# Kernel optimization log

Measured on AMD Instinct MI355X. Metric: run time of the kernel, lower is better.

## Reference

```python
import jax, jax.numpy as jnp
import numpy as np

PROP_TIME = 3
# (top,bottom),(left,right) zero-pad widths for the 8 neighbor shifts,
# matching torch ZeroPad2d((left,right,top,bottom)) in the original module.
PADS = [((0, 2), (0, 2)), ((0, 2), (1, 1)), ((0, 2), (2, 0)),
        ((1, 1), (0, 2)),                   ((1, 1), (2, 0)),
        ((2, 0), (0, 2)), ((2, 0), (1, 1)), ((2, 0), (2, 0))]


def _pad8(x, axis):
    """Pad last two dims 8 ways, stack the copies on `axis`."""
    lead = [(0, 0)] * (x.ndim - 2)
    return jnp.stack([jnp.pad(x, lead + [tb, lr]) for (tb, lr) in PADS], axis=axis)


def _affinity_norm(g):
    # g: [N, 8, H, W] -> gate_wb [N, 8, H+2, W+2], gate_sum [N, H, W]
    gw = jnp.stack([jnp.pad(g[:, k], [(0, 0), PADS[k][0], PADS[k][1]])
                    for k in range(8)], axis=1)
    abs_w = jnp.sum(jnp.abs(gw), axis=1, keepdims=True)
    gw = gw / abs_w
    gsum = jnp.sum(gw, axis=1)[:, 1:-1, 1:-1]
    return gw, gsum


def _propagate_once(gw, gsum, blur):
    # gw: [N,8,H+2,W+2], gsum: [N,H,W], blur: [N,B,H,W]
    nb = _pad8(blur, axis=1)                                # [N,8,B,H+2,W+2]
    ws = jnp.sum(gw[:, :, None] * nb, axis=1)[:, :, 1:-1, 1:-1]  # [N,B,H,W]
    return (1.0 - gsum[:, None]) * blur + ws


def _forward(guidance, blur, prop_time):
    # guidance: [24, X, Y, Z], blur: [B, X, Y, Z]
    gwx, gsx = _affinity_norm(jnp.transpose(guidance[0:8],   (3, 0, 1, 2)))  # [Z,8,X,Y]
    gwy, gsy = _affinity_norm(jnp.transpose(guidance[8:16],  (2, 0, 1, 3)))  # [Y,8,X,Z]
    gwz, gsz = _affinity_norm(jnp.transpose(guidance[16:24], (1, 0, 2, 3)))  # [X,8,Y,Z]
    r = blur
    for _ in range(prop_time):
        r = jnp.transpose(_propagate_once(gwx, gsx, jnp.transpose(r, (3, 0, 1, 2))), (1, 2, 3, 0))
        r = jnp.transpose(_propagate_once(gwy, gsy, jnp.transpose(r, (2, 0, 1, 3))), (1, 2, 0, 3))
        r = jnp.transpose(_propagate_once(gwz, gsz, jnp.transpose(r, (1, 0, 2, 3))), (1, 0, 2, 3))
    return r


def setup_inputs() -> dict:
    key = jax.random.key(0)
    k1, k2 = jax.random.split(key)
    guidance = jax.random.normal(k1, (24, 256, 256, 32), dtype=jnp.float32)
    blur = jax.random.normal(k2, (1, 256, 256, 32), dtype=jnp.float32)
    return {"guidance": guidance, "blur": blur}


def reference(guidance, blur):
    return _forward(guidance, blur, PROP_TIME)
```

## Files before the change

kernel.cpp:

```cpp
#include <hip/hip_runtime.h>


constexpr int X = 256, Y = 256, Z = 32;
constexpr int NV = X * Y * Z;
constexpr int YZ = Y * Z;

__device__ __forceinline__ float4 zero4() { return make_float4(0.f, 0.f, 0.f, 0.f); }

__device__ __forceinline__ void accum(const float4 gk, const float4 rk,
                                      float* asum, float* gsum, float* acc) {
    asum[0] += fabsf(gk.x); gsum[0] += gk.x; acc[0] = fmaf(gk.x, rk.x, acc[0]);
    asum[1] += fabsf(gk.y); gsum[1] += gk.y; acc[1] = fmaf(gk.y, rk.y, acc[1]);
    asum[2] += fabsf(gk.z); gsum[2] += gk.z; acc[2] = fmaf(gk.z, rk.z, acc[2]);
    asum[3] += fabsf(gk.w); gsum[3] += gk.w; acc[3] = fmaf(gk.w, rk.w, acc[3]);
}

template <int DIR>
__global__ __launch_bounds__(256) void prop4(const float* __restrict__ g,
                                             const float* __restrict__ rin,
                                             float* __restrict__ rout) {
    const int t  = blockIdx.x * 256 + threadIdx.x;
    const int f0 = t << 2;
    const int z  = f0 & (Z - 1);
    const int y  = (f0 >> 5) & (Y - 1);
    const int x  = f0 >> 13;

    constexpr int d1[8] = {1, 1, 1, 0, 0, -1, -1, -1};
    constexpr int d2[8] = {1, 0, -1, 1, -1, 1, 0, -1};

    const float* gc = g + DIR * 8 * NV;
    const float4 rc = *(const float4*)(rin + f0);
    float asum[4] = {0, 0, 0, 0}, gsum[4] = {0, 0, 0, 0}, acc[4] = {0, 0, 0, 0};

    if (DIR == 0) {
#pragma unroll
        for (int k = 0; k < 8; ++k) {
            const int a = x + d1[k], b = y + d2[k];
            if (a >= 0 && a < X && b >= 0 && b < Y) {
                const int ofs = f0 + d1[k] * YZ + d2[k] * Z;
                const float4 gv = *(const float4*)(gc + k * NV + ofs);
                const float4 rv = *(const float4*)(rin + ofs);
                accum(gv, rv, asum, gsum, acc);
            }
        }
    } else {
        const int s1 = (DIR == 1) ? YZ : Z;
        const int c1 = (DIR == 1) ? x : y;

        float4 rv[3]; float rl[3], rr[3];
#pragma unroll
        for (int j = 0; j < 3; ++j) {
            const int dd = 1 - j;
            const bool v = (c1 + dd >= 0) && (c1 + dd < 256);
            const float* p = rin + f0 + dd * s1;
            rv[j] = v ? *(const float4*)p : zero4();
            rl[j] = (v && z > 0)     ? p[-1] : 0.f;
            rr[j] = (v && z < Z - 4) ? p[4]  : 0.f;
        }

#pragma unroll
        for (int k = 0; k < 8; ++k) {
            const int j = 1 - d1[k];
            const bool v = (c1 + d1[k] >= 0) && (c1 + d1[k] < 256);
            const float* p = gc + k * NV + f0 + d1[k] * s1;
            const float4 gv = v ? *(const float4*)p : zero4();
            float4 gk, rk;
            if (d2[k] == 1) {
                const float s = (v && z < Z - 4) ? p[4] : 0.f;
                gk = make_float4(gv.y, gv.z, gv.w, s);
                rk = make_float4(rv[j].y, rv[j].z, rv[j].w, rr[j]);
            } else if (d2[k] == -1) {
                const float s = (v && z > 0) ? p[-1] : 0.f;
                gk = make_float4(s, gv.x, gv.y, gv.z);
                rk = make_float4(rl[j], rv[j].x, rv[j].y, rv[j].z);
            } else {
                gk = gv; rk = rv[j];
            }
            accum(gk, rk, asum, gsum, acc);
        }
    }

    float4 o;
    o.x = rc.x + (acc[0] - gsum[0] * rc.x) / asum[0];
    o.y = rc.y + (acc[1] - gsum[1] * rc.y) / asum[1];
    o.z = rc.z + (acc[2] - gsum[2] * rc.z) / asum[2];
    o.w = rc.w + (acc[3] - gsum[3] * rc.w) / asum[3];
    *(float4*)(rout + f0) = o;
}

extern "C" void kernel_launch(void* const* d_in, const int* in_sizes, int n_in,
                              void* d_out, int out_size, void* d_ws, size_t ws_size,
                              hipStream_t stream) {
    const float* g    = (const float*)d_in[0];
    const float* blur = (const float*)d_in[1];
    float* out = (float*)d_out;
    float* ws  = (float*)d_ws;

    const dim3 grid(NV / 1024), block(256);

    const float* src = blur;
    int step = 0;
    for (int it = 0; it < 3; ++it) {
        for (int dir = 0; dir < 3; ++dir) {
            float* dst = (step & 1) ? ws : out;
            switch (dir) {
                case 0: prop4<0><<<grid, block, 0, stream>>>(g, src, dst); break;
                case 1: prop4<1><<<grid, block, 0, stream>>>(g, src, dst); break;
                case 2: prop4<2><<<grid, block, 0, stream>>>(g, src, dst); break;
            }
            src = dst;
            ++step;
        }
    }
}
```

Measured before the change: 375.3 us.

## Fuse nine propagation launches into one cooperative kernel with grid sync

Replaces the nine separate per-direction kernel launches with a single cooperative kernel of 256 blocks that loops over all steps, separated by grid-wide syncs, and falls back to per-step launches if the cooperative launch fails. Conditional loads become clamped unconditional loads with masking, the accumulation is rewritten as g*(r_neighbor - r_center) so the separate gate sum is dropped, and division is replaced by a hardware reciprocal. The goal is to remove launch overhead and branchy memory access, but only 256 blocks with one block per CU limits occupancy for a memory-bound stencil, and the approximate reciprocal slightly changes numerics.

After: 872.3 us. 132% more time.

```diff
diff --git a/kernel.cpp b/kernel.cpp
--- a/kernel.cpp
+++ b/kernel.cpp
@@ -1,91 +1,134 @@
 #include <hip/hip_runtime.h>
+#include <hip/hip_cooperative_groups.h>
+
+namespace cg = cooperative_groups;
 
 
 constexpr int X = 256, Y = 256, Z = 32;
 constexpr int NV = X * Y * Z;
 constexpr int YZ = Y * Z;
+constexpr int GEND = 24 * NV;
 
-__device__ __forceinline__ float4 zero4() { return make_float4(0.f, 0.f, 0.f, 0.f); }
-
-__device__ __forceinline__ void accum(const float4 gk, const float4 rk,
-                                      float* asum, float* gsum, float* acc) {
-    asum[0] += fabsf(gk.x); gsum[0] += gk.x; acc[0] = fmaf(gk.x, rk.x, acc[0]);
-    asum[1] += fabsf(gk.y); gsum[1] += gk.y; acc[1] = fmaf(gk.y, rk.y, acc[1]);
-    asum[2] += fabsf(gk.z); gsum[2] += gk.z; acc[2] = fmaf(gk.z, rk.z, acc[2]);
-    asum[3] += fabsf(gk.w); gsum[3] += gk.w; acc[3] = fmaf(gk.w, rk.w, acc[3]);
+__device__ __forceinline__ int iclamp(int v, int lo, int hi) {
+    return min(max(v, lo), hi);
 }
 
 template <int DIR>
-__global__ __launch_bounds__(256) void prop4(const float* __restrict__ g,
-                                             const float* __restrict__ rin,
-                                             float* __restrict__ rout) {
-    const int t  = blockIdx.x * 256 + threadIdx.x;
-    const int f0 = t << 2;
-    const int z  = f0 & (Z - 1);
-    const int y  = (f0 >> 5) & (Y - 1);
-    const int x  = f0 >> 13;
-
+__device__ __forceinline__ void do_group(int f0, const float* __restrict__ g,
+                                         const float* __restrict__ src,
+                                         float* __restrict__ dst) {
     constexpr int d1[8] = {1, 1, 1, 0, 0, -1, -1, -1};
     constexpr int d2[8] = {1, 0, -1, 1, -1, 1, 0, -1};
+    const int z = f0 & 31, y = (f0 >> 5) & 255, x = f0 >> 13;
+    const int gb0 = DIR * 8 * NV;
 
-    const float* gc = g + DIR * 8 * NV;
-    const float4 rc = *(const float4*)(rin + f0);
-    float asum[4] = {0, 0, 0, 0}, gsum[4] = {0, 0, 0, 0}, acc[4] = {0, 0, 0, 0};
+    float asx = 0, asy = 0, asz = 0, asw = 0;
+    float dx = 0, dy = 0, dz = 0, dw = 0;
+    float4 rc;
 
     if (DIR == 0) {
+        rc = *(const float4*)(src + f0);
 #pragma unroll
         for (int k = 0; k < 8; ++k) {
             const int a = x + d1[k], b = y + d2[k];
-            if (a >= 0 && a < X && b >= 0 && b < Y) {
-                const int ofs = f0 + d1[k] * YZ + d2[k] * Z;
-                const float4 gv = *(const float4*)(gc + k * NV + ofs);
-                const float4 rv = *(const float4*)(rin + ofs);
-                accum(gv, rv, asum, gsum, acc);
-            }
+            const bool valid = ((unsigned)a < 256u) & ((unsigned)b < 256u);
+            const int ofs = f0 + d1[k] * YZ + d2[k] * Z;
+            const float4 rv = *(const float4*)(src + iclamp(ofs, 0, NV - 4));
+            float4 gv = *(const float4*)(g + iclamp(gb0 + k * NV + ofs, 0, GEND - 4));
+            if (!valid) { gv.x = 0.f; gv.y = 0.f; gv.z = 0.f; gv.w = 0.f; }
+            asx += fabsf(gv.x); asy += fabsf(gv.y);
+            asz += fabsf(gv.z); asw += fabsf(gv.w);
+            dx = fmaf(gv.x, rv.x - rc.x, dx); dy = fmaf(gv.y, rv.y - rc.y, dy);
+            dz = fmaf(gv.z, rv.z - rc.z, dz); dw = fmaf(gv.w, rv.w - rc.w, dw);
         }
     } else {
         const int s1 = (DIR == 1) ? YZ : Z;
         const int c1 = (DIR == 1) ? x : y;
-
         float4 rv[3]; float rl[3], rr[3];
 #pragma unroll
         for (int j = 0; j < 3; ++j) {
-            const int dd = 1 - j;
-            const bool v = (c1 + dd >= 0) && (c1 + dd < 256);
-            const float* p = rin + f0 + dd * s1;
-            rv[j] = v ? *(const float4*)p : zero4();
-            rl[j] = (v && z > 0)     ? p[-1] : 0.f;
-            rr[j] = (v && z < Z - 4) ? p[4]  : 0.f;
+            const int ro = f0 + (1 - j) * s1;
+            rv[j] = *(const float4*)(src + iclamp(ro, 0, NV - 4));
+            rl[j] = src[iclamp(ro - 1, 0, NV - 1)];
+            rr[j] = src[iclamp(ro + 4, 0, NV - 1)];
         }
-
+        rc = rv[1];
+        const bool zlo = (z > 0), zhi = (z < Z - 4);
 #pragma unroll
         for (int k = 0; k < 8; ++k) {
             const int j = 1 - d1[k];
-            const bool v = (c1 + d1[k] >= 0) && (c1 + d1[k] < 256);
-            const float* p = gc + k * NV + f0 + d1[k] * s1;
-            const float4 gv = v ? *(const float4*)p : zero4();
+            const bool vrow = (unsigned)(c1 + d1[k]) < 256u;
+            const int gb = gb0 + k * NV + f0 + d1[k] * s1;
+            float4 gv = *(const float4*)(g + iclamp(gb, 0, GEND - 4));
+            if (!vrow) { gv.x = 0.f; gv.y = 0.f; gv.z = 0.f; gv.w = 0.f; }
             float4 gk, rk;
             if (d2[k] == 1) {
-                const float s = (v && z < Z - 4) ? p[4] : 0.f;
-                gk = make_float4(gv.y, gv.z, gv.w, s);
+                float ge = g[iclamp(gb + 4, 0, GEND - 1)];
+                ge = (vrow && zhi) ? ge : 0.f;
+                gk = make_float4(gv.y, gv.z, gv.w, ge);
                 rk = make_float4(rv[j].y, rv[j].z, rv[j].w, rr[j]);
             } else if (d2[k] == -1) {
-                const float s = (v && z > 0) ? p[-1] : 0.f;
-                gk = make_float4(s, gv.x, gv.y, gv.z);
+                float ge = g[iclamp(gb - 1, 0, GEND - 1)];
+                ge = (vrow && zlo) ? ge : 0.f;
+                gk = make_float4(ge, gv.x, gv.y, gv.z);
                 rk = make_float4(rl[j], rv[j].x, rv[j].y, rv[j].z);
             } else {
                 gk = gv; rk = rv[j];
             }
-            accum(gk, rk, asum, gsum, acc);
+            asx += fabsf(gk.x); asy += fabsf(gk.y);
+            asz += fabsf(gk.z); asw += fabsf(gk.w);
+            dx = fmaf(gk.x, rk.x - rc.x, dx); dy = fmaf(gk.y, rk.y - rc.y, dy);
+            dz = fmaf(gk.z, rk.z - rc.z, dz); dw = fmaf(gk.w, rk.w - rc.w, dw);
         }
     }
 
     float4 o;
-    o.x = rc.x + (acc[0] - gsum[0] * rc.x) / asum[0];
-    o.y = rc.y + (acc[1] - gsum[1] * rc.y) / asum[1];
-    o.z = rc.z + (acc[2] - gsum[2] * rc.z) / asum[2];
-    o.w = rc.w + (acc[3] - gsum[3] * rc.w) / asum[3];
-    *(float4*)(rout + f0) = o;
+    o.x = rc.x + dx * __builtin_amdgcn_rcpf(asx);
+    o.y = rc.y + dy * __builtin_amdgcn_rcpf(asy);
+    o.z = rc.z + dz * __builtin_amdgcn_rcpf(asz);
+    o.w = rc.w + dw * __builtin_amdgcn_rcpf(asw);
+    *(float4*)(dst + f0) = o;
+}
+
+constexpr int NTH = 256 * 256;
+constexpr int GRP = NV / 4 / NTH;
+
+__global__ __launch_bounds__(256, 1) void prop_all(const float* __restrict__ g,
+                                                   const float* __restrict__ blur,
+                                                   float* __restrict__ bufA,
+                                                   float* __restrict__ bufB,
+                                                   float* __restrict__ out) {
+    cg::grid_group grid = cg::this_grid();
+    const int u = blockIdx.x * 256 + threadIdx.x;
+
+    for (int step = 0; step < 9; ++step) {
+        const float* src = (step == 0) ? blur : ((step & 1) ? bufA : bufB);
+        float* dst = (step == 8) ? out : ((step & 1) ? bufB : bufA);
+        const int dir = step % 3;
+
+        if (dir == 0) {
+#pragma unroll 2
+            for (int j = 0; j < GRP; ++j) do_group<0>((u + j * NTH) << 2, g, src, dst);
+        } else if (dir == 1) {
+#pragma unroll 2
+            for (int j = 0; j < GRP; ++j) do_group<1>((u + j * NTH) << 2, g, src, dst);
+        } else {
+#pragma unroll 2
+            for (int j = 0; j < GRP; ++j) do_group<2>((u + j * NTH) << 2, g, src, dst);
+        }
+        if (step < 8) {
+            __threadfence();
+            grid.sync();
+        }
+    }
+}
+
+template <int DIR>
+__global__ __launch_bounds__(256) void prop_step(const float* __restrict__ g,
+                                                 const float* __restrict__ rin,
+                                                 float* __restrict__ rout) {
+    const int t = blockIdx.x * 256 + threadIdx.x;
+    do_group<DIR>(t << 2, g, rin, rout);
 }
 
 extern "C" void kernel_launch(void* const* d_in, const int* in_sizes, int n_in,
@@ -93,23 +136,26 @@
                               hipStream_t stream) {
     const float* g    = (const float*)d_in[0];
     const float* blur = (const float*)d_in[1];
-    float* out = (float*)d_out;
-    float* ws  = (float*)d_ws;
+    float* out  = (float*)d_out;
+    float* bufA = (float*)d_ws;
+    float* bufB = bufA + NV;
 
-    const dim3 grid(NV / 1024), block(256);
-
-    const float* src = blur;
-    int step = 0;
-    for (int it = 0; it < 3; ++it) {
-        for (int dir = 0; dir < 3; ++dir) {
-            float* dst = (step & 1) ? ws : out;
-            switch (dir) {
-                case 0: prop4<0><<<grid, block, 0, stream>>>(g, src, dst); break;
-                case 1: prop4<1><<<grid, block, 0, stream>>>(g, src, dst); break;
-                case 2: prop4<2><<<grid, block, 0, stream>>>(g, src, dst); break;
+    void* args[] = {(void*)&g, (void*)&blur, (void*)&bufA, (void*)&bufB, (void*)&out};
+    hipError_t err = hipLaunchCooperativeKernel((void*)prop_all, dim3(256), dim3(256),
+                                                args, 0, stream);
+    if (err != hipSuccess) {
+        (void)hipGetLastError();
+        const dim3 grid(NV / 1024), block(256);
+        const float* src = blur;
+        for (int step = 0; step < 9; ++step) {
+            float* dst = (step == 8) ? out : ((step & 1) ? bufB : bufA);
+            if (step < 8) dst = (step & 1) ? bufB : bufA;
+            switch (step % 3) {
+                case 0: prop_step<0><<<grid, block, 0, stream>>>(g, src, dst); break;
+                case 1: prop_step<1><<<grid, block, 0, stream>>>(g, src, dst); break;
+                case 2: prop_step<2><<<grid, block, 0, stream>>>(g, src, dst); break;
             }
             src = dst;
-            ++step;
         }
     }
 }
```
